# Optimization experiments

Measured on AMD Instinct MI355X. Metric: run time of the kernel, lower is better.

The kernel has to match this reference:

```python
import jax, jax.numpy as jnp
import numpy as np


def _bilinear_resample(imgs, dvfs):
    # imgs: (B,H,W,C), dvfs: (B,H,W,2) with channel 0 = x(width) offset, 1 = y(height) offset
    B, H, W, C = imgs.shape
    fx = jnp.arange(W, dtype=imgs.dtype)[None, None, :] + dvfs[..., 0]  # (B,H,W)
    fy = jnp.arange(H, dtype=imgs.dtype)[None, :, None] + dvfs[..., 1]  # (B,H,W)

    x0f = jnp.floor(fx)
    y0f = jnp.floor(fy)
    wx = fx - x0f  # fractional weights
    wy = fy - y0f
    x0 = x0f.astype(jnp.int32)
    y0 = y0f.astype(jnp.int32)
    x1 = x0 + 1
    y1 = y0 + 1

    def gather(iy, ix):
        # zero-padding semantics for out-of-bounds corners (tf resampler behavior)
        valid = (ix >= 0) & (ix < W) & (iy >= 0) & (iy < H)
        ixc = jnp.clip(ix, 0, W - 1)
        iyc = jnp.clip(iy, 0, H - 1)
        vals = jax.vmap(lambda im, yy, xx: im[yy, xx])(imgs, iyc, ixc)  # (B,H,W,C)
        return vals * valid[..., None].astype(imgs.dtype)

    v00 = gather(y0, x0)
    v01 = gather(y0, x1)
    v10 = gather(y1, x0)
    v11 = gather(y1, x1)

    wx = wx[..., None]
    wy = wy[..., None]
    return (v00 * (1 - wx) * (1 - wy)
            + v01 * wx * (1 - wy)
            + v10 * (1 - wx) * wy
            + v11 * wx * wy)


def setup_inputs() -> dict:
    key = jax.random.key(0)
    k1, k2 = jax.random.split(key)
    B, H, W = 32, 1024, 1024
    imgs = jax.random.normal(k1, (B, H, W, 1), dtype=jnp.float32)
    dvfs = jax.random.normal(k2, (B, H, W, 2), dtype=jnp.float32)
    return {"imgs": imgs, "dvfs": dvfs}


def reference(imgs, dvfs):
    return _bilinear_resample(imgs, dvfs)
```

## Files before the change

### kernel.cpp

```cpp
#include <hip/hip_runtime.h>
#include <hip/hip_bf16.h>


#define H_DIM 1024
#define W_DIM 1024

__device__ __forceinline__ float gather_zp(const float* __restrict__ img,
                                           int yy, int xx) {
    bool valid = (xx >= 0) & (xx < W_DIM) & (yy >= 0) & (yy < H_DIM);
    int xc = min(max(xx, 0), W_DIM - 1);
    int yc = min(max(yy, 0), H_DIM - 1);
    float v = img[yc * W_DIM + xc];
    return valid ? v : 0.0f;
}

__global__ __launch_bounds__(256) void bilerp_kernel(
        const float* __restrict__ imgs,
        const float* __restrict__ dvfs,
        float* __restrict__ out,
        long long total_pixels) {
    long long tid = (long long)blockIdx.x * blockDim.x + threadIdx.x;
    long long base = tid * 4;
    if (base >= total_pixels) return;

    const int hw = H_DIM * W_DIM;
    int b   = (int)(base / hw);
    int rem = (int)(base % hw);
    int y   = rem / W_DIM;
    int x   = rem % W_DIM;

    const float* __restrict__ img = imgs + (long long)b * hw;

    const float4* dvf4 = (const float4*)(dvfs + base * 2);
    float4 d0 = dvf4[0];
    float4 d1 = dvf4[1];
    float dx[4] = {d0.x, d0.z, d1.x, d1.z};
    float dy[4] = {d0.y, d0.w, d1.y, d1.w};

    float4 res;
    float* rp = &res.x;
    #pragma unroll
    for (int i = 0; i < 4; ++i) {
        float fx = (float)(x + i) + dx[i];
        float fy = (float)y       + dy[i];
        float x0f = floorf(fx);
        float y0f = floorf(fy);
        float wx = fx - x0f;
        float wy = fy - y0f;
        int x0 = (int)x0f;
        int y0 = (int)y0f;
        int x1 = x0 + 1;
        int y1 = y0 + 1;

        float v00 = gather_zp(img, y0, x0);
        float v01 = gather_zp(img, y0, x1);
        float v10 = gather_zp(img, y1, x0);
        float v11 = gather_zp(img, y1, x1);

        rp[i] = v00 * (1.0f - wx) * (1.0f - wy)
              + v01 * wx          * (1.0f - wy)
              + v10 * (1.0f - wx) * wy
              + v11 * wx          * wy;
    }

    *(float4*)(out + base) = res;
}

extern "C" void kernel_launch(void* const* d_in, const int* in_sizes, int n_in,
                              void* d_out, int out_size, void* d_ws, size_t ws_size,
                              hipStream_t stream) {
    const float* imgs = (const float*)d_in[0];
    const float* dvfs = (const float*)d_in[1];
    float* out = (float*)d_out;

    long long total_pixels = (long long)out_size;
    long long n_threads = (total_pixels + 3) / 4;
    int block = 256;
    long long grid = (n_threads + block - 1) / block;

    bilerp_kernel<<<(dim3)(unsigned)grid, block, 0, stream>>>(imgs, dvfs, out, total_pixels);
}
```

Baseline: 530.3 us.

## Map one pixel per thread with nontemporal dvf loads and output stores

Switches from four pixels per thread using float4 loads and stores to one pixel per thread, reading each displacement pair as a 64-bit nontemporal load and writing each output with a nontemporal store. Index math moves to 32-bit shifts and masks instead of 64-bit division. The aim is more threads in flight to hide gather latency, and keeping streamed dvf and output data from evicting image lines that the gathers reuse in cache. The trade-off is four times as many threads and narrower per-thread memory transactions.

```diff
diff --git a/kernel.cpp b/kernel.cpp
--- a/kernel.cpp
+++ b/kernel.cpp
@@ -1,9 +1,10 @@
 #include <hip/hip_runtime.h>
-#include <hip/hip_bf16.h>
 
 
 #define H_DIM 1024
 #define W_DIM 1024
+#define HW_SHIFT 20
+#define HW_PIX (1 << HW_SHIFT)
 
 __device__ __forceinline__ float gather_zp(const float* __restrict__ img,
                                            int yy, int xx) {
@@ -18,52 +19,43 @@
         const float* __restrict__ imgs,
         const float* __restrict__ dvfs,
         float* __restrict__ out,
-        long long total_pixels) {
-    long long tid = (long long)blockIdx.x * blockDim.x + threadIdx.x;
-    long long base = tid * 4;
-    if (base >= total_pixels) return;
+        int total_pixels) {
+    int pix = blockIdx.x * 256 + threadIdx.x;
+    if (pix >= total_pixels) return;
 
-    const int hw = H_DIM * W_DIM;
-    int b   = (int)(base / hw);
-    int rem = (int)(base % hw);
-    int y   = rem / W_DIM;
-    int x   = rem % W_DIM;
+    int b   = pix >> HW_SHIFT;
+    int rem = pix & (HW_PIX - 1);
+    int y   = rem >> 10;
+    int x   = rem & (W_DIM - 1);
 
-    const float* __restrict__ img = imgs + (long long)b * hw;
+    const float* __restrict__ img = imgs + ((long long)b << HW_SHIFT);
 
-    const float4* dvf4 = (const float4*)(dvfs + base * 2);
-    float4 d0 = dvf4[0];
-    float4 d1 = dvf4[1];
-    float dx[4] = {d0.x, d0.z, d1.x, d1.z};
-    float dy[4] = {d0.y, d0.w, d1.y, d1.w};
+    union { double d64; float2 f2; } cvt;
+    cvt.d64 = __builtin_nontemporal_load(
+        reinterpret_cast<const double*>(dvfs) + pix);
+    float dx = cvt.f2.x;
+    float dy = cvt.f2.y;
 
-    float4 res;
-    float* rp = &res.x;
-    #pragma unroll
-    for (int i = 0; i < 4; ++i) {
-        float fx = (float)(x + i) + dx[i];
-        float fy = (float)y       + dy[i];
-        float x0f = floorf(fx);
-        float y0f = floorf(fy);
-        float wx = fx - x0f;
-        float wy = fy - y0f;
-        int x0 = (int)x0f;
-        int y0 = (int)y0f;
-        int x1 = x0 + 1;
-        int y1 = y0 + 1;
+    float fx = (float)x + dx;
+    float fy = (float)y + dy;
+    float x0f = floorf(fx);
+    float y0f = floorf(fy);
+    float wx = fx - x0f;
+    float wy = fy - y0f;
+    int x0 = (int)x0f;
+    int y0 = (int)y0f;
 
-        float v00 = gather_zp(img, y0, x0);
-        float v01 = gather_zp(img, y0, x1);
-        float v10 = gather_zp(img, y1, x0);
-        float v11 = gather_zp(img, y1, x1);
+    float v00 = gather_zp(img, y0,     x0);
+    float v01 = gather_zp(img, y0,     x0 + 1);
+    float v10 = gather_zp(img, y0 + 1, x0);
+    float v11 = gather_zp(img, y0 + 1, x0 + 1);
 
-        rp[i] = v00 * (1.0f - wx) * (1.0f - wy)
+    float res = v00 * (1.0f - wx) * (1.0f - wy)
               + v01 * wx          * (1.0f - wy)
               + v10 * (1.0f - wx) * wy
               + v11 * wx          * wy;
-    }
 
-    *(float4*)(out + base) = res;
+    __builtin_nontemporal_store(res, out + pix);
 }
 
 extern "C" void kernel_launch(void* const* d_in, const int* in_sizes, int n_in,
@@ -73,10 +65,9 @@
     const float* dvfs = (const float*)d_in[1];
     float* out = (float*)d_out;
 
-    long long total_pixels = (long long)out_size;
-    long long n_threads = (total_pixels + 3) / 4;
+    int total_pixels = out_size;
     int block = 256;
-    long long grid = (n_threads + block - 1) / block;
+    int grid = (total_pixels + block - 1) / block;
 
-    bilerp_kernel<<<(dim3)(unsigned)grid, block, 0, stream>>>(imgs, dvfs, out, total_pixels);
+    bilerp_kernel<<<grid, block, 0, stream>>>(imgs, dvfs, out, total_pixels);
 }
```

Measured after the change: 505.9 us. -4.6%, faster.
